# Performance work log

Hardware: AMD Instinct MI355X
Metric: run time of the kernel (lower is better)

The kernel has to match this reference:

```python
import jax, jax.numpy as jnp
import numpy as np

N_NODES = 100000
N_EDGES = 600000
IN_DIM = 128
HID = 128
N_GRAPHS = 512
N_CLASSES = 10


def setup_inputs() -> dict:
    key = jax.random.key(0)
    ks = jax.random.split(key, 8)
    feats = jax.random.normal(ks[0], (N_NODES, IN_DIM), dtype=jnp.float32)
    W = jax.random.normal(ks[1], (IN_DIM, HID), dtype=jnp.float32) * 0.05
    b = jnp.zeros((HID,), dtype=jnp.float32)
    W1 = jax.random.normal(ks[2], (HID, 12), dtype=jnp.float32) * 0.05
    b1 = jnp.zeros((12,), dtype=jnp.float32)
    W2 = jax.random.normal(ks[3], (12, N_CLASSES), dtype=jnp.float32) * 0.05
    b2 = jnp.zeros((N_CLASSES,), dtype=jnp.float32)
    src = jax.random.randint(ks[4], (N_EDGES,), 0, N_NODES, dtype=jnp.int32)
    dst = jax.random.randint(ks[5], (N_EDGES,), 0, N_NODES, dtype=jnp.int32)
    graph_ids = jnp.sort(jax.random.randint(ks[6], (N_NODES,), 0, N_GRAPHS, dtype=jnp.int32))
    return {"feats": feats, "W": W, "b": b, "W1": W1, "b1": b1, "W2": W2,
            "b2": b2, "src": src, "dst": dst, "graph_ids": graph_ids}


def reference(feats, W, b, W1, b1, W2, b2, src, dst, graph_ids):
    ones_e = jnp.ones((src.shape[0],), dtype=feats.dtype)
    # DGL GraphConv norm='both': clamp degrees to >= 1
    out_deg = jnp.maximum(jax.ops.segment_sum(ones_e, src, num_segments=N_NODES), 1.0)
    in_deg = jnp.maximum(jax.ops.segment_sum(ones_e, dst, num_segments=N_NODES), 1.0)
    norm_src = out_deg ** -0.5  # [N]
    norm_dst = in_deg ** -0.5
    x = feats * norm_src[:, None]               # scale source features
    agg = jax.ops.segment_sum(x[src], dst, num_segments=N_NODES)  # gather-scatter SpMM
    h = agg * norm_dst[:, None]
    h = jnp.maximum(h @ W + b, 0.0)             # GraphConv linear + ReLU  [N, HID]
    # mean_nodes: per-graph segment mean (empty graphs -> 0, matching DGL)
    gsum = jax.ops.segment_sum(h, graph_ids, num_segments=N_GRAPHS)
    cnt = jax.ops.segment_sum(jnp.ones((N_NODES,), h.dtype), graph_ids, num_segments=N_GRAPHS)
    hg = jnp.where(cnt[:, None] > 0, gsum / jnp.maximum(cnt, 1.0)[:, None], 0.0)
    # tiny 2-layer MLP classifier
    return (hg @ W1 + b1) @ W2 + b2             # [N_GRAPHS, N_CLASSES]
```

## Files before the change

### kernel.cpp

```cpp
#include <hip/hip_runtime.h>
#include <hip/hip_fp16.h>

#define N_NODES 100000
#define N_EDGES 600000
#define DIM 128
#define N_GRAPHS 512
#define MLP_HID 12
#define N_CLASSES 10
#define NPB 16
#define SLOT_CAP 32
#define TPAD 136
#define EPT 4

#define WFRAG_BLOCKS 8
#define EDGE_BLOCKS ((N_EDGES + 256*EPT - 1) / (256*EPT))
#define CONV_BLOCKS 6250
#define NBLK (N_NODES / NPB)

typedef _Float16 half8 __attribute__((ext_vector_type(8)));
typedef float float4v __attribute__((ext_vector_type(4)));
typedef float floatx2 __attribute__((ext_vector_type(2)));

__global__ void prep_kernel(const int* __restrict__ src, const int* __restrict__ dst,
                            int* __restrict__ out_hist, int* __restrict__ in_hist,
                            int* __restrict__ slots,
                            const float* __restrict__ W, __half* __restrict__ wfrag,
                            const float4* __restrict__ feats4, int2* __restrict__ feats_q) {
    int bx = blockIdx.x;
    if (bx < WFRAG_BLOCKS) {
        int item = bx * 256 + threadIdx.x;
        if (item < 2048) {
            int lane = item & 63;
            int kt = (item >> 6) & 3;
            int nt = item >> 8;
            int n = nt * 16 + (lane & 15);
            int k0 = kt * 32 + (lane >> 4) * 8;
            union { int4 i4; __half h[8]; } u;
            #pragma unroll
            for (int j = 0; j < 8; ++j) u.h[j] = __float2half(W[(k0 + j) * DIM + n]);
            ((int4*)wfrag)[item] = u.i4;
        }
        return;
    }
    if (bx < WFRAG_BLOCKS + EDGE_BLOCKS) {
        int base = (bx - WFRAG_BLOCKS) * (256 * EPT) + threadIdx.x;
        int s[EPT], d[EPT]; bool ok[EPT];
        #pragma unroll
        for (int e = 0; e < EPT; ++e) {
            int i = base + e * 256;
            ok[e] = (i < N_EDGES);
            s[e] = ok[e] ? src[i] : 0;
            d[e] = ok[e] ? dst[i] : 0;
        }
        #pragma unroll
        for (int e = 0; e < EPT; ++e) if (ok[e]) atomicAdd(&out_hist[s[e]], 1);
        int tk[EPT];
        #pragma unroll
        for (int e = 0; e < EPT; ++e) tk[e] = ok[e] ? atomicAdd(&in_hist[d[e]], 1) : SLOT_CAP;
        #pragma unroll
        for (int e = 0; e < EPT; ++e)
            if (tk[e] < SLOT_CAP) slots[d[e] * SLOT_CAP + tk[e]] = s[e];
        return;
    }
    int i = (bx - WFRAG_BLOCKS - EDGE_BLOCKS) * 256 + threadIdx.x;
    float4 a = feats4[2 * i];
    float4 c = feats4[2 * i + 1];
    int lo = __builtin_amdgcn_cvt_pk_fp8_f32(a.x, a.y, 0, false);
    lo     = __builtin_amdgcn_cvt_pk_fp8_f32(a.z, a.w, lo, true);
    int hi = __builtin_amdgcn_cvt_pk_fp8_f32(c.x, c.y, 0, false);
    hi     = __builtin_amdgcn_cvt_pk_fp8_f32(c.z, c.w, hi, true);
    feats_q[i] = make_int2(lo, hi);
}

__global__ __launch_bounds__(128) void fused_gemm(
        const int* __restrict__ feats_q,
        const int* __restrict__ in_hist, const int* __restrict__ out_hist,
        const int* __restrict__ slots,
        const __half* __restrict__ wfrag,
        const float* __restrict__ bvec, const int* __restrict__ gid,
        float* __restrict__ partial, __half* __restrict__ mixed_h) {
    __shared__ __half tile_h[NPB][TPAD];
    int t = threadIdx.x;
    int group = t >> 5;
    int lane = t & 31;
    int node0 = blockIdx.x * NPB;

    int dv = 0;
    if (lane < 16) dv = in_hist[node0 + lane];
    int deg[4]; int es[4]; float nsf[4];
    #pragma unroll
    for (int r = 0; r < 4; ++r) {
        int j = r * 4 + group;
        deg[r] = __shfl(dv, j, 32);
        int m = min(deg[r], SLOT_CAP);
        es[r] = 0;
        if (lane < m) es[r] = slots[(node0 + j) * SLOT_CAP + lane];
        nsf[r] = 0.f;
        if (lane < m) nsf[r] = rsqrtf((float)max(out_hist[es[r]], 1));
    }

    #pragma unroll
    for (int r = 0; r < 4; ++r) {
        int j = r * 4 + group;
        int m = min(deg[r], SLOT_CAP);
        float4 a4 = make_float4(0.f, 0.f, 0.f, 0.f);
        int i = 0;
        for (; i + 4 <= m; i += 4) {
            int sn0 = __shfl(es[r], i + 0, 32), sn1 = __shfl(es[r], i + 1, 32);
            int sn2 = __shfl(es[r], i + 2, 32), sn3 = __shfl(es[r], i + 3, 32);
            float ns0 = __shfl(nsf[r], i + 0, 32), ns1 = __shfl(nsf[r], i + 1, 32);
            float ns2 = __shfl(nsf[r], i + 2, 32), ns3 = __shfl(nsf[r], i + 3, 32);
            int q0 = feats_q[sn0 * 32 + lane];
            int q1 = feats_q[sn1 * 32 + lane];
            int q2 = feats_q[sn2 * 32 + lane];
            int q3 = feats_q[sn3 * 32 + lane];
            floatx2 p0 = __builtin_amdgcn_cvt_pk_f32_fp8(q0, false);
            floatx2 r0 = __builtin_amdgcn_cvt_pk_f32_fp8(q0, true);
            floatx2 p1 = __builtin_amdgcn_cvt_pk_f32_fp8(q1, false);
            floatx2 r1 = __builtin_amdgcn_cvt_pk_f32_fp8(q1, true);
            floatx2 p2 = __builtin_amdgcn_cvt_pk_f32_fp8(q2, false);
            floatx2 r2 = __builtin_amdgcn_cvt_pk_f32_fp8(q2, true);
            floatx2 p3 = __builtin_amdgcn_cvt_pk_f32_fp8(q3, false);
            floatx2 r3 = __builtin_amdgcn_cvt_pk_f32_fp8(q3, true);
            a4.x = fmaf(p0[0], ns0, fmaf(p1[0], ns1, fmaf(p2[0], ns2, fmaf(p3[0], ns3, a4.x))));
            a4.y = fmaf(p0[1], ns0, fmaf(p1[1], ns1, fmaf(p2[1], ns2, fmaf(p3[1], ns3, a4.y))));
            a4.z = fmaf(r0[0], ns0, fmaf(r1[0], ns1, fmaf(r2[0], ns2, fmaf(r3[0], ns3, a4.z))));
            a4.w = fmaf(r0[1], ns0, fmaf(r1[1], ns1, fmaf(r2[1], ns2, fmaf(r3[1], ns3, a4.w))));
        }
        for (; i < m; ++i) {
            int sn = __shfl(es[r], i, 32);
            float nsv = __shfl(nsf[r], i, 32);
            int q = feats_q[sn * 32 + lane];
            floatx2 p = __builtin_amdgcn_cvt_pk_f32_fp8(q, false);
            floatx2 rr = __builtin_amdgcn_cvt_pk_f32_fp8(q, true);
            a4.x = fmaf(p[0], nsv, a4.x);
            a4.y = fmaf(p[1], nsv, a4.y);
            a4.z = fmaf(rr[0], nsv, a4.z);
            a4.w = fmaf(rr[1], nsv, a4.w);
        }
        float nd = rsqrtf((float)max(deg[r], 1));
        union { int2 v; __half2 h2[2]; } st;
        st.h2[0] = __floats2half2_rn(a4.x * nd, a4.y * nd);
        st.h2[1] = __floats2half2_rn(a4.z * nd, a4.w * nd);
        *(int2*)&tile_h[j][lane * 4] = st.v;
    }
    __syncthreads();

    int wave = t >> 6;
    int wl = t & 63;
    int quad = wl >> 4;
    int col = wl & 15;

    half8 afrag[4];
    #pragma unroll
    for (int kt = 0; kt < 4; ++kt)
        afrag[kt] = *reinterpret_cast<const half8*>(&tile_h[col][kt * 32 + quad * 8]);

    float4v c[4];
    #pragma unroll
    for (int nt = 0; nt < 4; ++nt) { c[nt][0] = 0.f; c[nt][1] = 0.f; c[nt][2] = 0.f; c[nt][3] = 0.f; }

    #pragma unroll
    for (int nt = 0; nt < 4; ++nt) {
        int ntile = wave * 4 + nt;
        #pragma unroll
        for (int kt = 0; kt < 4; ++kt) {
            half8 bfrag = *reinterpret_cast<const half8*>(wfrag + ((size_t)(ntile * 4 + kt) * 64 + wl) * 8);
            c[nt] = __builtin_amdgcn_mfma_f32_16x16x32_f16(afrag[kt], bfrag, c[nt], 0, 0, 0);
        }
    }

    int g0 = gid[node0];
    if (gid[node0 + NPB - 1] == g0) {
        #pragma unroll
        for (int nt = 0; nt < 4; ++nt) {
            float bb = bvec[(wave * 4 + nt) * 16 + col];
            float v = 0.f;
            #pragma unroll
            for (int i2 = 0; i2 < 4; ++i2) v += fmaxf(c[nt][i2] + bb, 0.f);
            v += __shfl_xor(v, 16, 64);
            v += __shfl_xor(v, 32, 64);
            if (wl < 16) partial[blockIdx.x * DIM + (wave * 4 + nt) * 16 + col] = v;
        }
    } else {
        #pragma unroll
        for (int nt = 0; nt < 4; ++nt) {
            float bb = bvec[(wave * 4 + nt) * 16 + col];
            #pragma unroll
            for (int i2 = 0; i2 < 4; ++i2)
                mixed_h[(size_t)blockIdx.x * (NPB * DIM) + (quad * 4 + i2) * DIM
                        + (wave * 4 + nt) * 16 + col] = __float2half(fmaxf(c[nt][i2] + bb, 0.f));
        }
    }
}

__device__ __forceinline__ int lower_bound_i(const int* __restrict__ a, int n, int v) {
    int lo = 0, hi = n;
    while (lo < hi) { int mid = (lo + hi) >> 1; if (a[mid] < v) lo = mid + 1; else hi = mid; }
    return lo;
}

__global__ __launch_bounds__(128) void mlp_kernel(
        const float* __restrict__ partial, const __half* __restrict__ mixed_h,
        const int* __restrict__ gid,
        const float* __restrict__ W1, const float* __restrict__ b1,
        const float* __restrict__ W2, const float* __restrict__ b2,
        float* __restrict__ out) {
    __shared__ float s[DIM];
    __shared__ float t1[MLP_HID];
    int g = blockIdx.x;
    int t = threadIdx.x;
    int s_g = lower_bound_i(gid, N_NODES, g);
    int e_g = lower_bound_i(gid, N_NODES, g + 1);
    float cntf = (float)(e_g - s_g);
    float acc = 0.f;
    int b_lo = (s_g + NPB - 1) >> 4;
    int b_hi = e_g >> 4;
    if (b_lo < b_hi) {
        for (int b = b_lo; b < b_hi; ++b) acc += partial[b * DIM + t];
        for (int n = s_g; n < b_lo * NPB; ++n)
            acc += __half2float(mixed_h[(size_t)(n >> 4) * (NPB * DIM) + (n & 15) * DIM + t]);
        for (int n = b_hi * NPB; n < e_g; ++n)
            acc += __half2float(mixed_h[(size_t)(n >> 4) * (NPB * DIM) + (n & 15) * DIM + t]);
    } else {
        for (int n = s_g; n < e_g; ++n)
            acc += __half2float(mixed_h[(size_t)(n >> 4) * (NPB * DIM) + (n & 15) * DIM + t]);
    }
    s[t] = (cntf > 0.f) ? (acc / cntf) : 0.f;
    __syncthreads();
    if (t < MLP_HID) {
        float a = b1[t];
        for (int k = 0; k < DIM; ++k) a = fmaf(s[k], W1[k * MLP_HID + t], a);
        t1[t] = a;
    }
    __syncthreads();
    if (t < N_CLASSES) {
        float o = b2[t];
        #pragma unroll
        for (int j = 0; j < MLP_HID; ++j) o = fmaf(t1[j], W2[j * N_CLASSES + t], o);
        out[g * N_CLASSES + t] = o;
    }
}

extern "C" void kernel_launch(void* const* d_in, const int* in_sizes, int n_in,
                              void* d_out, int out_size, void* d_ws, size_t ws_size,
                              hipStream_t stream) {
    const float* feats = (const float*)d_in[0];
    const float* W     = (const float*)d_in[1];
    const float* b     = (const float*)d_in[2];
    const float* W1    = (const float*)d_in[3];
    const float* b1    = (const float*)d_in[4];
    const float* W2    = (const float*)d_in[5];
    const float* b2    = (const float*)d_in[6];
    const int*   src   = (const int*)d_in[7];
    const int*   dst   = (const int*)d_in[8];
    const int*   gid   = (const int*)d_in[9];
    float* out = (float*)d_out;

    char* ws = (char*)d_ws;
    int*   out_hist = (int*)ws;   ws += (size_t)N_NODES * 4;
    int*   in_hist  = (int*)ws;   ws += (size_t)N_NODES * 4;
    size_t zero_bytes = (size_t)(ws - (char*)d_ws);
    ws = (char*)(((uintptr_t)ws + 255) & ~(uintptr_t)255);
    int*    slots   = (int*)ws;    ws += (size_t)N_NODES * SLOT_CAP * 4;
    int*    feats_q = (int*)ws;    ws += (size_t)N_NODES * DIM;
    __half* wfrag   = (__half*)ws; ws += (size_t)2048 * 8 * 2;
    ws = (char*)(((uintptr_t)ws + 255) & ~(uintptr_t)255);
    float*  partial = (float*)ws;  ws += (size_t)NBLK * DIM * 4;
    __half* mixed_h = (__half*)ws; ws += (size_t)NBLK * NPB * DIM * 2;

    hipMemsetAsync(d_ws, 0, zero_bytes, stream);

    prep_kernel<<<WFRAG_BLOCKS + EDGE_BLOCKS + CONV_BLOCKS, 256, 0, stream>>>(
        src, dst, out_hist, in_hist, slots, W, wfrag, (const float4*)feats, (int2*)feats_q);

    fused_gemm<<<NBLK, 128, 0, stream>>>(
        feats_q, in_hist, out_hist, slots, wfrag, b, gid, partial, mixed_h);

    mlp_kernel<<<N_GRAPHS, 128, 0, stream>>>(partial, mixed_h, gid, W1, b1, W2, b2, out);
}
```

Measured before the change: 202.0 us.

## Build degree histograms per node-range in shared memory, drop memset

Replaces global-atomic degree counting with 125 blocks that each own a range of 800 nodes. Every block scans the full edge list and counts in shared-memory atomics, then writes its histogram range directly. This removes the workspace memset and the contended global atomics. In exchange, each of the 125 blocks rereads all 600K src/dst entries, so edge-list traffic is multiplied and the work per block is long and serial.

```diff
diff --git a/kernel.cpp b/kernel.cpp
--- a/kernel.cpp
+++ b/kernel.cpp
@@ -10,12 +10,12 @@
 #define NPB 16
 #define SLOT_CAP 32
 #define TPAD 136
-#define EPT 4
-
+#define NBLK (N_NODES / NPB)
+
+#define NPN 800
+#define EDGE_SCAN_BLOCKS (N_NODES / NPN)
 #define WFRAG_BLOCKS 8
-#define EDGE_BLOCKS ((N_EDGES + 256*EPT - 1) / (256*EPT))
 #define CONV_BLOCKS 6250
-#define NBLK (N_NODES / NPB)
 
 typedef _Float16 half8 __attribute__((ext_vector_type(8)));
 typedef float float4v __attribute__((ext_vector_type(4)));
@@ -42,27 +42,38 @@
         }
         return;
     }
-    if (bx < WFRAG_BLOCKS + EDGE_BLOCKS) {
-        int base = (bx - WFRAG_BLOCKS) * (256 * EPT) + threadIdx.x;
-        int s[EPT], d[EPT]; bool ok[EPT];
-        #pragma unroll
-        for (int e = 0; e < EPT; ++e) {
-            int i = base + e * 256;
-            ok[e] = (i < N_EDGES);
-            s[e] = ok[e] ? src[i] : 0;
-            d[e] = ok[e] ? dst[i] : 0;
-        }
-        #pragma unroll
-        for (int e = 0; e < EPT; ++e) if (ok[e]) atomicAdd(&out_hist[s[e]], 1);
-        int tk[EPT];
-        #pragma unroll
-        for (int e = 0; e < EPT; ++e) tk[e] = ok[e] ? atomicAdd(&in_hist[d[e]], 1) : SLOT_CAP;
-        #pragma unroll
-        for (int e = 0; e < EPT; ++e)
-            if (tk[e] < SLOT_CAP) slots[d[e] * SLOT_CAP + tk[e]] = s[e];
+    if (bx < WFRAG_BLOCKS + EDGE_SCAN_BLOCKS) {
+        __shared__ int cnt_in[NPN];
+        __shared__ int cnt_out[NPN];
+        int base = (bx - WFRAG_BLOCKS) * NPN;
+        for (int k = threadIdx.x; k < NPN; k += 256) { cnt_in[k] = 0; cnt_out[k] = 0; }
+        __syncthreads();
+        const int4* src4 = (const int4*)src;
+        const int4* dst4 = (const int4*)dst;
+        for (int i = threadIdx.x; i < N_EDGES / 4; i += 256) {
+            int4 s4 = src4[i];
+            int4 d4 = dst4[i];
+            int ss[4] = { s4.x, s4.y, s4.z, s4.w };
+            int dd[4] = { d4.x, d4.y, d4.z, d4.w };
+            #pragma unroll
+            for (int e = 0; e < 4; ++e) {
+                unsigned so = (unsigned)(ss[e] - base);
+                if (so < NPN) atomicAdd(&cnt_out[so], 1);
+                unsigned dofs = (unsigned)(dd[e] - base);
+                if (dofs < NPN) {
+                    int tk = atomicAdd(&cnt_in[dofs], 1);
+                    if (tk < SLOT_CAP) slots[dd[e] * SLOT_CAP + tk] = ss[e];
+                }
+            }
+        }
+        __syncthreads();
+        for (int k = threadIdx.x; k < NPN; k += 256) {
+            out_hist[base + k] = cnt_out[k];
+            in_hist[base + k] = cnt_in[k];
+        }
         return;
     }
-    int i = (bx - WFRAG_BLOCKS - EDGE_BLOCKS) * 256 + threadIdx.x;
+    int i = (bx - WFRAG_BLOCKS - EDGE_SCAN_BLOCKS) * 256 + threadIdx.x;
     float4 a = feats4[2 * i];
     float4 c = feats4[2 * i + 1];
     int lo = __builtin_amdgcn_cvt_pk_fp8_f32(a.x, a.y, 0, false);
@@ -260,7 +271,6 @@
     char* ws = (char*)d_ws;
     int*   out_hist = (int*)ws;   ws += (size_t)N_NODES * 4;
     int*   in_hist  = (int*)ws;   ws += (size_t)N_NODES * 4;
-    size_t zero_bytes = (size_t)(ws - (char*)d_ws);
     ws = (char*)(((uintptr_t)ws + 255) & ~(uintptr_t)255);
     int*    slots   = (int*)ws;    ws += (size_t)N_NODES * SLOT_CAP * 4;
     int*    feats_q = (int*)ws;    ws += (size_t)N_NODES * DIM;
@@ -269,9 +279,7 @@
     float*  partial = (float*)ws;  ws += (size_t)NBLK * DIM * 4;
     __half* mixed_h = (__half*)ws; ws += (size_t)NBLK * NPB * DIM * 2;
 
-    hipMemsetAsync(d_ws, 0, zero_bytes, stream);
-
-    prep_kernel<<<WFRAG_BLOCKS + EDGE_BLOCKS + CONV_BLOCKS, 256, 0, stream>>>(
+    prep_kernel<<<WFRAG_BLOCKS + EDGE_SCAN_BLOCKS + CONV_BLOCKS, 256, 0, stream>>>(
         src, dst, out_hist, in_hist, slots, W, wfrag, (const float4*)feats, (int2*)feats_q);
 
     fused_gemm<<<NBLK, 128, 0, stream>>>(
```

New measurement: 424.2 us. 110% more time.

## Apply weight GEMM before aggregation and gather transformed fp8 features

Applied to the files above, without the earlier changes.

Reorders the computation so each node's features are multiplied by W first (X·W is done in the prep kernel with MFMA, then quantized to fp8), and the gather kernel then sums transformed rows, adding bias and ReLU before pooling. This moves the GEMM off the gather kernel's critical path and overlaps it with the edge-histogram blocks. The memset is replaced by an init kernel that zeros the histograms and builds the weight fragments. The fp8 quantization now applies to XW instead of X, which changes rounding error.

```diff
diff --git a/kernel.cpp b/kernel.cpp
--- a/kernel.cpp
+++ b/kernel.cpp
@@ -10,40 +10,46 @@
 #define NPB 16
 #define SLOT_CAP 32
 #define TPAD 136
+#define YPAD 132
 #define EPT 4
-
-#define WFRAG_BLOCKS 8
+#define NBLK (N_NODES / NPB)
+
 #define EDGE_BLOCKS ((N_EDGES + 256*EPT - 1) / (256*EPT))
-#define CONV_BLOCKS 6250
-#define NBLK (N_NODES / NPB)
+#define GEMM_BLOCKS (NBLK / 2)
+#define INIT_ZERO_BLOCKS ((2 * N_NODES + 255) / 256)
 
 typedef _Float16 half8 __attribute__((ext_vector_type(8)));
 typedef float float4v __attribute__((ext_vector_type(4)));
 typedef float floatx2 __attribute__((ext_vector_type(2)));
 
+__global__ void init_kernel(const float* __restrict__ W, __half* __restrict__ wfrag,
+                            int* __restrict__ hists ) {
+    int bx = blockIdx.x;
+    if (bx < 8) {
+        int item = bx * 256 + threadIdx.x;
+        int lane = item & 63;
+        int kt = (item >> 6) & 3;
+        int nt = item >> 8;
+        int n = nt * 16 + (lane & 15);
+        int k0 = kt * 32 + (lane >> 4) * 8;
+        union { int4 i4; __half h[8]; } u;
+        #pragma unroll
+        for (int j = 0; j < 8; ++j) u.h[j] = __float2half(W[(k0 + j) * DIM + n]);
+        ((int4*)wfrag)[item] = u.i4;
+        return;
+    }
+    int i = (bx - 8) * 256 + threadIdx.x;
+    if (i < 2 * N_NODES) hists[i] = 0;
+}
+
 __global__ void prep_kernel(const int* __restrict__ src, const int* __restrict__ dst,
                             int* __restrict__ out_hist, int* __restrict__ in_hist,
                             int* __restrict__ slots,
-                            const float* __restrict__ W, __half* __restrict__ wfrag,
-                            const float4* __restrict__ feats4, int2* __restrict__ feats_q) {
+                            const __half* __restrict__ wfrag,
+                            const float4* __restrict__ feats4, int* __restrict__ yq) {
     int bx = blockIdx.x;
-    if (bx < WFRAG_BLOCKS) {
-        int item = bx * 256 + threadIdx.x;
-        if (item < 2048) {
-            int lane = item & 63;
-            int kt = (item >> 6) & 3;
-            int nt = item >> 8;
-            int n = nt * 16 + (lane & 15);
-            int k0 = kt * 32 + (lane >> 4) * 8;
-            union { int4 i4; __half h[8]; } u;
-            #pragma unroll
-            for (int j = 0; j < 8; ++j) u.h[j] = __float2half(W[(k0 + j) * DIM + n]);
-            ((int4*)wfrag)[item] = u.i4;
-        }
-        return;
-    }
-    if (bx < WFRAG_BLOCKS + EDGE_BLOCKS) {
-        int base = (bx - WFRAG_BLOCKS) * (256 * EPT) + threadIdx.x;
+    if (bx < EDGE_BLOCKS) {
+        int base = bx * (256 * EPT) + threadIdx.x;
         int s[EPT], d[EPT]; bool ok[EPT];
         #pragma unroll
         for (int e = 0; e < EPT; ++e) {
@@ -62,24 +68,86 @@
             if (tk[e] < SLOT_CAP) slots[d[e] * SLOT_CAP + tk[e]] = s[e];
         return;
     }
-    int i = (bx - WFRAG_BLOCKS - EDGE_BLOCKS) * 256 + threadIdx.x;
-    float4 a = feats4[2 * i];
-    float4 c = feats4[2 * i + 1];
-    int lo = __builtin_amdgcn_cvt_pk_fp8_f32(a.x, a.y, 0, false);
-    lo     = __builtin_amdgcn_cvt_pk_fp8_f32(a.z, a.w, lo, true);
-    int hi = __builtin_amdgcn_cvt_pk_fp8_f32(c.x, c.y, 0, false);
-    hi     = __builtin_amdgcn_cvt_pk_fp8_f32(c.z, c.w, hi, true);
-    feats_q[i] = make_int2(lo, hi);
-}
-
-__global__ __launch_bounds__(128) void fused_gemm(
-        const int* __restrict__ feats_q,
+    __shared__ __half tile_h[2][NPB][TPAD];
+    __shared__ float ytile[2][NPB][YPAD];
+    int tid = threadIdx.x;
+    int u = tid >> 7;
+    int t = tid & 127;
+    int tile = (bx - EDGE_BLOCKS) * 2 + u;
+    int node0 = tile * NPB;
+
+    #pragma unroll
+    for (int it = 0; it < 4; ++it) {
+        int f = it * 128 + t;
+        int node = f >> 5;
+        int k4 = f & 31;
+        float4 v = feats4[(size_t)(node0 + node) * 32 + k4];
+        union { int2 q; __half2 h[2]; } st;
+        st.h[0] = __floats2half2_rn(v.x, v.y);
+        st.h[1] = __floats2half2_rn(v.z, v.w);
+        *(int2*)&tile_h[u][node][k4 * 4] = st.q;
+    }
+    __syncthreads();
+
+    int wave = t >> 6;
+    int wl = t & 63;
+    int quad = wl >> 4;
+    int col = wl & 15;
+
+    half8 afrag[4];
+    #pragma unroll
+    for (int kt = 0; kt < 4; ++kt)
+        afrag[kt] = *reinterpret_cast<const half8*>(&tile_h[u][col][kt * 32 + quad * 8]);
+
+    float4v c[4];
+    #pragma unroll
+    for (int nt = 0; nt < 4; ++nt) { c[nt][0] = 0.f; c[nt][1] = 0.f; c[nt][2] = 0.f; c[nt][3] = 0.f; }
+
+    #pragma unroll
+    for (int nt = 0; nt < 4; ++nt) {
+        int ntile = wave * 4 + nt;
+        #pragma unroll
+        for (int kt = 0; kt < 4; ++kt) {
+            half8 bfrag = *reinterpret_cast<const half8*>(wfrag + ((size_t)(ntile * 4 + kt) * 64 + wl) * 8);
+            c[nt] = __builtin_amdgcn_mfma_f32_16x16x32_f16(afrag[kt], bfrag, c[nt], 0, 0, 0);
+        }
+    }
+
+    #pragma unroll
+    for (int nt = 0; nt < 4; ++nt) {
+        #pragma unroll
+        for (int i2 = 0; i2 < 4; ++i2)
+            ytile[u][quad * 4 + i2][(wave * 4 + nt) * 16 + col] = c[nt][i2];
+    }
+    __syncthreads();
+
+    {
+        int node = t >> 3;
+        int kg = t & 7;
+        const float* yr = &ytile[u][node][kg * 16];
+        float4 y0 = *(const float4*)(yr + 0);
+        float4 y1 = *(const float4*)(yr + 4);
+        float4 y2 = *(const float4*)(yr + 8);
+        float4 y3 = *(const float4*)(yr + 12);
+        int d0 = __builtin_amdgcn_cvt_pk_fp8_f32(y0.x, y0.y, 0, false);
+        d0     = __builtin_amdgcn_cvt_pk_fp8_f32(y0.z, y0.w, d0, true);
+        int d1 = __builtin_amdgcn_cvt_pk_fp8_f32(y1.x, y1.y, 0, false);
+        d1     = __builtin_amdgcn_cvt_pk_fp8_f32(y1.z, y1.w, d1, true);
+        int d2 = __builtin_amdgcn_cvt_pk_fp8_f32(y2.x, y2.y, 0, false);
+        d2     = __builtin_amdgcn_cvt_pk_fp8_f32(y2.z, y2.w, d2, true);
+        int d3 = __builtin_amdgcn_cvt_pk_fp8_f32(y3.x, y3.y, 0, false);
+        d3     = __builtin_amdgcn_cvt_pk_fp8_f32(y3.z, y3.w, d3, true);
+        *(int4*)&yq[(size_t)(node0 + node) * 32 + kg * 4] = make_int4(d0, d1, d2, d3);
+    }
+}
+
+__global__ __launch_bounds__(128) void gather_kernel(
+        const int* __restrict__ yq,
         const int* __restrict__ in_hist, const int* __restrict__ out_hist,
         const int* __restrict__ slots,
-        const __half* __restrict__ wfrag,
         const float* __restrict__ bvec, const int* __restrict__ gid,
         float* __restrict__ partial, __half* __restrict__ mixed_h) {
-    __shared__ __half tile_h[NPB][TPAD];
+    __shared__ float pl[2][DIM];
     int t = threadIdx.x;
     int group = t >> 5;
     int lane = t & 31;
@@ -98,6 +166,10 @@
         nsf[r] = 0.f;
         if (lane < m) nsf[r] = rsqrtf((float)max(out_hist[es[r]], 1));
     }
+
+    float4 bb = *(const float4*)&bvec[lane * 4];
+    bool uni = (gid[node0] == gid[node0 + NPB - 1]);
+    float4 pool = make_float4(0.f, 0.f, 0.f, 0.f);
 
     #pragma unroll
     for (int r = 0; r < 4; ++r) {
@@ -110,10 +182,10 @@
             int sn2 = __shfl(es[r], i + 2, 32), sn3 = __shfl(es[r], i + 3, 32);
             float ns0 = __shfl(nsf[r], i + 0, 32), ns1 = __shfl(nsf[r], i + 1, 32);
             float ns2 = __shfl(nsf[r], i + 2, 32), ns3 = __shfl(nsf[r], i + 3, 32);
-            int q0 = feats_q[sn0 * 32 + lane];
-            int q1 = feats_q[sn1 * 32 + lane];
-            int q2 = feats_q[sn2 * 32 + lane];
-            int q3 = feats_q[sn3 * 32 + lane];
+            int q0 = yq[sn0 * 32 + lane];
+            int q1 = yq[sn1 * 32 + lane];
+            int q2 = yq[sn2 * 32 + lane];
+            int q3 = yq[sn3 * 32 + lane];
             floatx2 p0 = __builtin_amdgcn_cvt_pk_f32_fp8(q0, false);
             floatx2 r0 = __builtin_amdgcn_cvt_pk_f32_fp8(q0, true);
             floatx2 p1 = __builtin_amdgcn_cvt_pk_f32_fp8(q1, false);
@@ -130,7 +202,7 @@
         for (; i < m; ++i) {
             int sn = __shfl(es[r], i, 32);
             float nsv = __shfl(nsf[r], i, 32);
-            int q = feats_q[sn * 32 + lane];
+            int q = yq[sn * 32 + lane];
             floatx2 p = __builtin_amdgcn_cvt_pk_f32_fp8(q, false);
             floatx2 rr = __builtin_amdgcn_cvt_pk_f32_fp8(q, true);
             a4.x = fmaf(p[0], nsv, a4.x);
@@ -139,58 +211,30 @@
             a4.w = fmaf(rr[1], nsv, a4.w);
         }
         float nd = rsqrtf((float)max(deg[r], 1));
-        union { int2 v; __half2 h2[2]; } st;
-        st.h2[0] = __floats2half2_rn(a4.x * nd, a4.y * nd);
-        st.h2[1] = __floats2half2_rn(a4.z * nd, a4.w * nd);
-        *(int2*)&tile_h[j][lane * 4] = st.v;
-    }
-    __syncthreads();
-
-    int wave = t >> 6;
-    int wl = t & 63;
-    int quad = wl >> 4;
-    int col = wl & 15;
-
-    half8 afrag[4];
-    #pragma unroll
-    for (int kt = 0; kt < 4; ++kt)
-        afrag[kt] = *reinterpret_cast<const half8*>(&tile_h[col][kt * 32 + quad * 8]);
-
-    float4v c[4];
-    #pragma unroll
-    for (int nt = 0; nt < 4; ++nt) { c[nt][0] = 0.f; c[nt][1] = 0.f; c[nt][2] = 0.f; c[nt][3] = 0.f; }
-
-    #pragma unroll
-    for (int nt = 0; nt < 4; ++nt) {
-        int ntile = wave * 4 + nt;
-        #pragma unroll
-        for (int kt = 0; kt < 4; ++kt) {
-            half8 bfrag = *reinterpret_cast<const half8*>(wfrag + ((size_t)(ntile * 4 + kt) * 64 + wl) * 8);
-            c[nt] = __builtin_amdgcn_mfma_f32_16x16x32_f16(afrag[kt], bfrag, c[nt], 0, 0, 0);
-        }
-    }
-
-    int g0 = gid[node0];
-    if (gid[node0 + NPB - 1] == g0) {
-        #pragma unroll
-        for (int nt = 0; nt < 4; ++nt) {
-            float bb = bvec[(wave * 4 + nt) * 16 + col];
-            float v = 0.f;
-            #pragma unroll
-            for (int i2 = 0; i2 < 4; ++i2) v += fmaxf(c[nt][i2] + bb, 0.f);
-            v += __shfl_xor(v, 16, 64);
-            v += __shfl_xor(v, 32, 64);
-            if (wl < 16) partial[blockIdx.x * DIM + (wave * 4 + nt) * 16 + col] = v;
-        }
-    } else {
-        #pragma unroll
-        for (int nt = 0; nt < 4; ++nt) {
-            float bb = bvec[(wave * 4 + nt) * 16 + col];
-            #pragma unroll
-            for (int i2 = 0; i2 < 4; ++i2)
-                mixed_h[(size_t)blockIdx.x * (NPB * DIM) + (quad * 4 + i2) * DIM
-                        + (wave * 4 + nt) * 16 + col] = __float2half(fmaxf(c[nt][i2] + bb, 0.f));
-        }
+        float4 h;
+        h.x = fmaxf(fmaf(a4.x, nd, bb.x), 0.f);
+        h.y = fmaxf(fmaf(a4.y, nd, bb.y), 0.f);
+        h.z = fmaxf(fmaf(a4.z, nd, bb.z), 0.f);
+        h.w = fmaxf(fmaf(a4.w, nd, bb.w), 0.f);
+        if (uni) {
+            pool.x += h.x; pool.y += h.y; pool.z += h.z; pool.w += h.w;
+        } else {
+            union { int2 v; __half2 h2[2]; } st;
+            st.h2[0] = __floats2half2_rn(h.x, h.y);
+            st.h2[1] = __floats2half2_rn(h.z, h.w);
+            *(int2*)&mixed_h[(size_t)blockIdx.x * (NPB * DIM) + j * DIM + lane * 4] = st.v;
+        }
+    }
+
+    if (uni) {
+        pool.x += __shfl_xor(pool.x, 32, 64);
+        pool.y += __shfl_xor(pool.y, 32, 64);
+        pool.z += __shfl_xor(pool.z, 32, 64);
+        pool.w += __shfl_xor(pool.w, 32, 64);
+        int wave = t >> 6, wl = t & 63;
+        if (wl < 32) *(float4*)&pl[wave][wl * 4] = pool;
+        __syncthreads();
+        if (t < DIM) partial[blockIdx.x * DIM + t] = pl[0][t] + pl[1][t];
     }
 }
 
@@ -260,22 +304,21 @@
     char* ws = (char*)d_ws;
     int*   out_hist = (int*)ws;   ws += (size_t)N_NODES * 4;
     int*   in_hist  = (int*)ws;   ws += (size_t)N_NODES * 4;
-    size_t zero_bytes = (size_t)(ws - (char*)d_ws);
     ws = (char*)(((uintptr_t)ws + 255) & ~(uintptr_t)255);
     int*    slots   = (int*)ws;    ws += (size_t)N_NODES * SLOT_CAP * 4;
-    int*    feats_q = (int*)ws;    ws += (size_t)N_NODES * DIM;
+    int*    yq      = (int*)ws;    ws += (size_t)N_NODES * DIM;
     __half* wfrag   = (__half*)ws; ws += (size_t)2048 * 8 * 2;
     ws = (char*)(((uintptr_t)ws + 255) & ~(uintptr_t)255);
     float*  partial = (float*)ws;  ws += (size_t)NBLK * DIM * 4;
     __half* mixed_h = (__half*)ws; ws += (size_t)NBLK * NPB * DIM * 2;
 
-    hipMemsetAsync(d_ws, 0, zero_bytes, stream);
-
-    prep_kernel<<<WFRAG_BLOCKS + EDGE_BLOCKS + CONV_BLOCKS, 256, 0, stream>>>(
-        src, dst, out_hist, in_hist, slots, W, wfrag, (const float4*)feats, (int2*)feats_q);
-
-    fused_gemm<<<NBLK, 128, 0, stream>>>(
-        feats_q, in_hist, out_hist, slots, wfrag, b, gid, partial, mixed_h);
+    init_kernel<<<8 + INIT_ZERO_BLOCKS, 256, 0, stream>>>(W, wfrag, out_hist);
+
+    prep_kernel<<<EDGE_BLOCKS + GEMM_BLOCKS, 256, 0, stream>>>(
+        src, dst, out_hist, in_hist, slots, wfrag, (const float4*)feats, yq);
+
+    gather_kernel<<<NBLK, 128, 0, stream>>>(
+        yq, in_hist, out_hist, slots, b, gid, partial, mixed_h);
 
     mlp_kernel<<<N_GRAPHS, 128, 0, stream>>>(partial, mixed_h, gid, W1, b1, W2, b2, out);
 }
```

After: 200.3 us. Within noise of the previous version (-0.8%).
